# Kernel tuning notes

Measured on AMD Instinct MI355X. Metric: run time of the kernel, lower is better.

## Reference

```python
import jax, jax.numpy as jnp
import numpy as np

HIDDEN = 4096
N_HEADS = 32
N_KV_HEADS = 8
HEAD_DIM = HIDDEN // N_HEADS  # 128
GROUPS = N_HEADS // N_KV_HEADS  # 4
ROPE_BASE = 10000.0
BATCH, SEQ = 1, 2048


def _rope_cos_sin(position_ids, dim, base):
    # position_ids: [b, s] int -> cos/sin [b, s, dim]
    inv_freq = 1.0 / (base ** (jnp.arange(0, dim, 2, dtype=jnp.float32) / dim))  # [dim/2]
    freqs = position_ids.astype(jnp.float32)[..., None] * inv_freq  # [b, s, dim/2]
    emb = jnp.concatenate([freqs, freqs], axis=-1)  # [b, s, dim]
    return jnp.cos(emb), jnp.sin(emb)


def _rotate_half(x):
    x1, x2 = jnp.split(x, 2, axis=-1)
    return jnp.concatenate([-x2, x1], axis=-1)


def setup_inputs() -> dict:
    key = jax.random.key(0)
    ks = jax.random.split(key, 8)
    s = 0.02
    return {
        'hidden_states': jax.random.normal(ks[0], (BATCH, SEQ, HIDDEN), dtype=jnp.float32),
        'position_ids': jnp.broadcast_to(jnp.arange(SEQ, dtype=jnp.int64), (BATCH, SEQ)),
        'Wq': jax.random.normal(ks[1], (HIDDEN, N_HEADS * HEAD_DIM), dtype=jnp.float32) * s,
        'bq': jax.random.normal(ks[2], (N_HEADS * HEAD_DIM,), dtype=jnp.float32) * s,
        'Wk': jax.random.normal(ks[3], (HIDDEN, N_KV_HEADS * HEAD_DIM), dtype=jnp.float32) * s,
        'bk': jax.random.normal(ks[4], (N_KV_HEADS * HEAD_DIM,), dtype=jnp.float32) * s,
        'Wv': jax.random.normal(ks[5], (HIDDEN, N_KV_HEADS * HEAD_DIM), dtype=jnp.float32) * s,
        'bv': jax.random.normal(ks[6], (N_KV_HEADS * HEAD_DIM,), dtype=jnp.float32) * s,
        'Wo': jax.random.normal(ks[7], (HIDDEN, HIDDEN), dtype=jnp.float32) * s,
    }


def reference(hidden_states, position_ids, Wq, bq, Wk, bk, Wv, bv, Wo):
    b, s, _ = hidden_states.shape
    # QKV projections (bias=True for q/k/v per module)
    q = hidden_states @ Wq + bq  # [b, s, H*d]
    k = hidden_states @ Wk + bk  # [b, s, Hk*d]
    v = hidden_states @ Wv + bv  # [b, s, Hk*d]
    q = q.reshape(b, s, N_HEADS, HEAD_DIM)
    k = k.reshape(b, s, N_KV_HEADS, HEAD_DIM)
    v = v.reshape(b, s, N_KV_HEADS, HEAD_DIM)

    # RoPE gathered by position_ids
    cos, sin = _rope_cos_sin(position_ids, HEAD_DIM, ROPE_BASE)  # [b, s, d]
    cos = cos[:, :, None, :]
    sin = sin[:, :, None, :]
    q = q * cos + _rotate_half(q) * sin
    k = k * cos + _rotate_half(k) * sin

    # GQA causal attention: group query heads over shared kv heads
    qg = q.reshape(b, s, N_KV_HEADS, GROUPS, HEAD_DIM)
    scale = 1.0 / jnp.sqrt(jnp.asarray(HEAD_DIM, dtype=q.dtype))
    scores = jnp.einsum('bqhgd,bkhd->bhgqk', qg, k) * scale  # [b, Hk, g, s, s]
    causal = jnp.tril(jnp.ones((s, s), dtype=bool))
    scores = jnp.where(causal, scores, jnp.finfo(scores.dtype).min)
    probs = jax.nn.softmax(scores, axis=-1)
    out = jnp.einsum('bhgqk,bkhd->bqhgd', probs, v)  # [b, s, Hk, g, d]
    out = out.reshape(b, s, HIDDEN)
    return out @ Wo  # o_proj, bias=False
```

## Files before the change

### kernel.cpp

```cpp
#include <hip/hip_runtime.h>
#include <hip/hip_bf16.h>

typedef __hip_bfloat16 bf16;
typedef __attribute__((ext_vector_type(8))) __bf16 bf16x8;
typedef __attribute__((ext_vector_type(4))) float f32x4;

#define SEQ 2048
#define HID 4096
#define NH 32
#define NKV 8
#define HD 128
#define KVDIM 1024
#define QKVN 6144

#define MiB (1024 * 1024)

__device__ __forceinline__ void gl_lds16(const void* g, void* lds) {
  __builtin_amdgcn_global_load_lds((const __attribute__((address_space(1))) void*)g,
                                   (__attribute__((address_space(3))) void*)lds,
                                   16, 0, 0);
}

__device__ __forceinline__ float unplo(unsigned u) { return __uint_as_float(u << 16); }
__device__ __forceinline__ float unphi(unsigned u) { return __uint_as_float(u & 0xffff0000u); }
__device__ __forceinline__ unsigned packbf(float a, float b) {
  bf16 t[2] = {__float2bfloat16(a), __float2bfloat16(b)};
  return *reinterpret_cast<unsigned*>(t);
}

__global__ void cvt_kernel(const float* __restrict__ in, bf16* __restrict__ out, int n) {
  int i = (blockIdx.x * blockDim.x + threadIdx.x) * 4;
  if (i >= n) return;
  float4 v = *reinterpret_cast<const float4*>(in + i);
  bf16 o[4] = {__float2bfloat16(v.x), __float2bfloat16(v.y),
               __float2bfloat16(v.z), __float2bfloat16(v.w)};
  *reinterpret_cast<short4*>(out + i) = *reinterpret_cast<const short4*>(o);
}

__global__ void concat_bias_kernel(const float* __restrict__ bq, const float* __restrict__ bk,
                                   const float* __restrict__ bv, float* __restrict__ o) {
  int i = blockIdx.x * blockDim.x + threadIdx.x;
  if (i >= QKVN) return;
  o[i] = (i < HID) ? bq[i] : (i < HID + KVDIM ? bk[i - HID] : bv[i - HID - KVDIM]);
}

__global__ void transpose_all_kernel(const float* __restrict__ Wq, const float* __restrict__ Wk,
                                     const float* __restrict__ Wv, const float* __restrict__ Wo,
                                     bf16* __restrict__ Wqkvt, bf16* __restrict__ Wot) {
  __shared__ float tile[32][33];
  int t = blockIdx.x;
  const float* in;
  bf16* out;
  int si, xt, yt;
  if (t < 16384)      { in = Wq; out = Wqkvt;                           si = HID;   xt = t & 127; yt = t >> 7; }
  else if (t < 20480) { t -= 16384; in = Wk; out = Wqkvt + (size_t)HID * HID;           si = KVDIM; xt = t & 31; yt = t >> 5; }
  else if (t < 24576) { t -= 20480; in = Wv; out = Wqkvt + (size_t)(HID + KVDIM) * HID; si = KVDIM; xt = t & 31; yt = t >> 5; }
  else                { t -= 24576; in = Wo; out = Wot;                 si = HID;   xt = t & 127; yt = t >> 7; }
  int c0 = xt * 32, r0 = yt * 32;
  int tx = threadIdx.x, ty = threadIdx.y;
#pragma unroll
  for (int i = 0; i < 32; i += 8)
    tile[ty + i][tx] = in[(size_t)(r0 + ty + i) * si + (c0 + tx)];
  __syncthreads();
#pragma unroll
  for (int i = 0; i < 32; i += 8)
    out[(size_t)(c0 + ty + i) * HID + (r0 + tx)] = __float2bfloat16(tile[tx][ty + i]);
}

__global__ void postqkv_kernel(const bf16* __restrict__ Ch, bf16* __restrict__ Qb,
                               bf16* __restrict__ Kb, bf16* __restrict__ Vt) {
  __shared__ float tile[32][33];
  int b = blockIdx.x;
  int tid = threadIdx.x;
  if (b < 10240) {
    bool isQ = (b < 8192);
    int idx = (isQ ? b : b - 8192) * 256 + tid;
    int j = idx & 31;
    int h = (idx >> 5) & (isQ ? 31 : 7);
    int s = idx >> (isQ ? 10 : 8);
    size_t bi = (size_t)s * QKVN + (isQ ? 0 : HID) + h * HD;
    unsigned u1 = *reinterpret_cast<const unsigned*>(Ch + bi + 2 * j);
    unsigned u2 = *reinterpret_cast<const unsigned*>(Ch + bi + 64 + 2 * j);
    float x1a = unplo(u1), x1b = unphi(u1);
    float x2a = unplo(u2), x2b = unphi(u2);
    float inv0 = __expf(-(float)(2 * j) * 0.14391156831212787f);
    float inv1 = __expf(-(float)(2 * j + 1) * 0.14391156831212787f);
    float sn0, cs0, sn1, cs1;
    __sincosf((float)s * inv0, &sn0, &cs0);
    __sincosf((float)s * inv1, &sn1, &cs1);
    size_t bo = (size_t)s * (isQ ? HID : KVDIM) + h * HD;
    bf16* Ob = isQ ? Qb : Kb;
    *reinterpret_cast<unsigned*>(Ob + bo + 2 * j) =
        packbf(x1a * cs0 - x2a * sn0, x1b * cs1 - x2b * sn1);
    *reinterpret_cast<unsigned*>(Ob + bo + 64 + 2 * j) =
        packbf(x2a * cs0 + x1a * sn0, x2b * cs1 + x1b * sn1);
  } else {
    int t = b - 10240;
    int xt = t & 31, yt = t >> 5;
    int tx = tid & 31, ty = tid >> 5;
#pragma unroll
    for (int i = 0; i < 32; i += 8)
      tile[ty + i][tx] = __bfloat162float(Ch[(size_t)(yt * 32 + ty + i) * QKVN + (HID + KVDIM) + xt * 32 + tx]);
    __syncthreads();
#pragma unroll
    for (int i = 0; i < 32; i += 8)
      Vt[(size_t)(xt * 32 + ty + i) * SEQ + (yt * 32 + tx)] = __float2bfloat16(tile[tx][ty + i]);
  }
}

#define BARRIER() __builtin_amdgcn_s_barrier()
#define LGKM0()                                          \
  {                                                      \
    asm volatile("s_waitcnt lgkmcnt(0)" ::: "memory");   \
    __builtin_amdgcn_sched_barrier(0);                   \
  }
#define MFMA_ACC(d, x, y) d = __builtin_amdgcn_mfma_f32_16x16x32_bf16(x, y, d, 0, 0, 0)

__global__ __launch_bounds__(512, 2) void qkvgemm_kernel(
    const bf16* __restrict__ A,
    const bf16* __restrict__ Bt,
    const float* __restrict__ bias,
    bf16* __restrict__ Ch) {
  __shared__ bf16 lds[2][448 * 64];
  const int blk = blockIdx.x;
  const int sw = (blk & 7) * 32 + (blk >> 3);
  const int bx = sw & 31, by = sw >> 5;
  const int n0 = bx * 192;
  const int m0 = by * 256;
  const int tid = threadIdx.x;
  const int lane = tid & 63;
  const int w = tid >> 6;
  const int wr = w >> 2, wc = w & 3;
  const int hig = lane >> 4;
  const int nt = HID / 64;

#define QSTAGE_A(buf, t)                                                          \
  {                                                                               \
    _Pragma("unroll")                                                             \
    for (int _c = 0; _c < 4; ++_c) {                                              \
      int _row = _c * 64 + w * 8 + (lane >> 3);                                   \
      int _ch = (lane & 7) ^ ((lane >> 3) & 7);                                   \
      gl_lds16(A + (size_t)(m0 + _row) * HID + (size_t)(t) * 64 + _ch * 8,        \
               &lds[buf][(_c * 64 + w * 8) * 64]);                                \
    }                                                                             \
  }
#define QSTAGE_B(buf, t)                                                          \
  {                                                                               \
    _Pragma("unroll")                                                             \
    for (int _c = 0; _c < 3; ++_c) {                                              \
      int _row = _c * 64 + w * 8 + (lane >> 3);                                   \
      int _ch = (lane & 7) ^ ((lane >> 3) & 7);                                   \
      gl_lds16(Bt + (size_t)(n0 + _row) * HID + (size_t)(t) * 64 + _ch * 8,       \
               &lds[buf][(256 + _c * 64 + w * 8) * 64]);                          \
    }                                                                             \
  }

  auto rdA = [&](int cur, int mi, int ks) {
    int rr = wr * 128 + mi * 16 + (lane & 15);
    int byt = rr * 128 + (((ks * 32 + hig * 8) * 2) ^ ((rr & 7) << 4));
    return *reinterpret_cast<const bf16x8*>(
        reinterpret_cast<const char*>(&lds[cur][0]) + byt);
  };
  auto rdB = [&](int cur, int ni, int ks) {
    int rr = wc * 48 + ni * 16 + (lane & 15);
    int byt = 32768 + rr * 128 + (((ks * 32 + hig * 8) * 2) ^ ((rr & 7) << 4));
    return *reinterpret_cast<const bf16x8*>(
        reinterpret_cast<const char*>(&lds[cur][0]) + byt);
  };

  f32x4 acc[8][3];
  const f32x4 z = {0.f, 0.f, 0.f, 0.f};
#pragma unroll
  for (int i = 0; i < 8; ++i)
#pragma unroll
    for (int j = 0; j < 3; ++j) acc[i][j] = z;

  QSTAGE_A(0, 0); QSTAGE_B(0, 0);
  QSTAGE_B(1, 1);
  asm volatile("s_waitcnt vmcnt(3)" ::: "memory");
  BARRIER();

  bf16x8 a[4][2], b[3][2];
  int cur = 0;
  for (int t = 0; t < nt; ++t, cur ^= 1) {
#pragma unroll
    for (int mi = 0; mi < 4; ++mi) { a[mi][0] = rdA(cur, mi, 0); a[mi][1] = rdA(cur, mi, 1); }
#pragma unroll
    for (int ni = 0; ni < 3; ++ni) { b[ni][0] = rdB(cur, ni, 0); b[ni][1] = rdB(cur, ni, 1); }
    if (t + 1 < nt) QSTAGE_A(cur ^ 1, t + 1);
    LGKM0();
    __builtin_amdgcn_s_setprio(1);
#pragma unroll
    for (int mi = 0; mi < 4; ++mi)
#pragma unroll
      for (int ni = 0; ni < 3; ++ni) {
        MFMA_ACC(acc[mi][ni], a[mi][0], b[ni][0]);
        MFMA_ACC(acc[mi][ni], a[mi][1], b[ni][1]);
      }
    __builtin_amdgcn_s_setprio(0);
    BARRIER();
#pragma unroll
    for (int mi = 0; mi < 4; ++mi) { a[mi][0] = rdA(cur, mi + 4, 0); a[mi][1] = rdA(cur, mi + 4, 1); }
    if (t + 2 < nt) QSTAGE_B(cur, t + 2);
    LGKM0();
    __builtin_amdgcn_s_setprio(1);
#pragma unroll
    for (int mi = 0; mi < 4; ++mi)
#pragma unroll
      for (int ni = 0; ni < 3; ++ni) {
        MFMA_ACC(acc[mi + 4][ni], a[mi][0], b[ni][0]);
        MFMA_ACC(acc[mi + 4][ni], a[mi][1], b[ni][1]);
      }
    __builtin_amdgcn_s_setprio(0);
    if (t + 1 < nt) {
      if (t + 2 < nt) {
        asm volatile("s_waitcnt vmcnt(3)" ::: "memory");
      } else {
        asm volatile("s_waitcnt vmcnt(0)" ::: "memory");
      }
    }
    BARRIER();
  }

#pragma unroll
  for (int ni = 0; ni < 3; ++ni) {
    int col = n0 + wc * 48 + ni * 16 + (lane & 15);
    float bv = bias[col];
#pragma unroll
    for (int mi = 0; mi < 8; ++mi) {
      int rbase = m0 + wr * 128 + mi * 16 + hig * 4;
#pragma unroll
      for (int r = 0; r < 4; ++r)
        Ch[(size_t)(rbase + r) * QKVN + col] = __float2bfloat16(acc[mi][ni][r] + bv);
    }
  }
#undef QSTAGE_A
#undef QSTAGE_B
}

__global__ __launch_bounds__(512, 2) void wogemm_kernel(
    const bf16* __restrict__ A,
    const bf16* __restrict__ Bt,
    float* __restrict__ C) {
  __shared__ bf16 lds[2][3][128 * 64];
  const int blk = blockIdx.x;
  const int sw = (blk & 7) * 32 + (blk >> 3);
  const int n0 = (sw & 31) * 128;
  const int m0 = (sw >> 5) * 256;
  const int tid = threadIdx.x;
  const int lane = tid & 63;
  const int w = tid >> 6;
  const int wr = w >> 1, wc = w & 1;
  const int nt = HID / 64;

#define WSTAGE(buf, slot, t)                                                    \
  {                                                                             \
    const bf16* _s = ((slot) == 2) ? Bt : A;                                    \
    int _g0 = ((slot) == 2) ? n0 : (m0 + (slot) * 128);                         \
    _Pragma("unroll")                                                           \
    for (int _it = 0; _it < 2; ++_it) {                                         \
      int _row = w * 16 + _it * 8 + (lane >> 3);                                \
      int _ch = (lane & 7) ^ (_row & 7);                                        \
      gl_lds16(_s + (size_t)(_g0 + _row) * HID + (size_t)(t) * 64 + _ch * 8,    \
               &lds[buf][slot][(w * 16 + _it * 8) * 64]);                       \
    }                                                                           \
  }

  auto rdA = [&](int cur, int mi, int ks) {
    int rr = (wr & 1) * 64 + mi * 16 + (lane & 15);
    int byt = rr * 128 + (((ks * 32 + (lane >> 4) * 8) * 2) ^ ((rr & 7) << 4));
    return *reinterpret_cast<const bf16x8*>(
        reinterpret_cast<const char*>(&lds[cur][wr >> 1][0]) + byt);
  };
  auto rdB = [&](int cur, int ni, int ks) {
    int rr = wc * 64 + ni * 16 + (lane & 15);
    int byt = rr * 128 + (((ks * 32 + (lane >> 4) * 8) * 2) ^ ((rr & 7) << 4));
    return *reinterpret_cast<const bf16x8*>(
        reinterpret_cast<const char*>(&lds[cur][2][0]) + byt);
  };

  f32x4 acc[4][4];
  const f32x4 z = {0.f, 0.f, 0.f, 0.f};
#pragma unroll
  for (int i = 0; i < 4; ++i)
#pragma unroll
    for (int j = 0; j < 4; ++j) acc[i][j] = z;

  WSTAGE(0, 0, 0); WSTAGE(0, 1, 0); WSTAGE(0, 2, 0);
  WSTAGE(1, 2, 1);
  asm volatile("s_waitcnt vmcnt(2)" ::: "memory");
  BARRIER();

  bf16x8 a[2][2], b[4][2];
  int cur = 0;
  for (int t = 0; t < nt; ++t, cur ^= 1) {
#pragma unroll
    for (int mi = 0; mi < 2; ++mi) { a[mi][0] = rdA(cur, mi, 0); a[mi][1] = rdA(cur, mi, 1); }
#pragma unroll
    for (int ni = 0; ni < 4; ++ni) { b[ni][0] = rdB(cur, ni, 0); b[ni][1] = rdB(cur, ni, 1); }
    if (t + 1 < nt) { WSTAGE(cur ^ 1, 0, t + 1); WSTAGE(cur ^ 1, 1, t + 1); }
    LGKM0();
    __builtin_amdgcn_s_setprio(1);
#pragma unroll
    for (int mi = 0; mi < 2; ++mi)
#pragma unroll
      for (int ni = 0; ni < 4; ++ni) {
        MFMA_ACC(acc[mi][ni], a[mi][0], b[ni][0]);
        MFMA_ACC(acc[mi][ni], a[mi][1], b[ni][1]);
      }
    __builtin_amdgcn_s_setprio(0);
    BARRIER();
#pragma unroll
    for (int mi = 0; mi < 2; ++mi) { a[mi][0] = rdA(cur, mi + 2, 0); a[mi][1] = rdA(cur, mi + 2, 1); }
    if (t + 2 < nt) WSTAGE(cur, 2, t + 2);
    LGKM0();
    __builtin_amdgcn_s_setprio(1);
#pragma unroll
    for (int mi = 0; mi < 2; ++mi)
#pragma unroll
      for (int ni = 0; ni < 4; ++ni) {
        MFMA_ACC(acc[mi + 2][ni], a[mi][0], b[ni][0]);
        MFMA_ACC(acc[mi + 2][ni], a[mi][1], b[ni][1]);
      }
    __builtin_amdgcn_s_setprio(0);
    if (t + 1 < nt) {
      if (t + 2 < nt) {
        asm volatile("s_waitcnt vmcnt(2)" ::: "memory");
      } else {
        asm volatile("s_waitcnt vmcnt(0)" ::: "memory");
      }
    }
    BARRIER();
  }

#pragma unroll
  for (int ni = 0; ni < 4; ++ni) {
    int col = n0 + wc * 64 + ni * 16 + (lane & 15);
#pragma unroll
    for (int mi = 0; mi < 4; ++mi) {
      int rbase = m0 + wr * 64 + mi * 16 + (lane >> 4) * 4;
#pragma unroll
      for (int r = 0; r < 4; ++r)
        C[(size_t)(rbase + r) * HID + col] = acc[mi][ni][r];
    }
  }
#undef WSTAGE
}

__global__ __launch_bounds__(256) void attn_kernel(
    const bf16* __restrict__ Q, const bf16* __restrict__ Kb,
    const bf16* __restrict__ Vt, bf16* __restrict__ AO,
    float* __restrict__ Opart, float* __restrict__ Ml) {
  __shared__ bf16 Ks[64 * 128];
  __shared__ bf16 Vs[128 * 64];
  __shared__ bf16 Ps[4][16 * 64];
  const int tid = threadIdx.x, lane = tid & 63, w = tid >> 6;
  const int b = blockIdx.x;
  const int H = b & 31;
  const int tt = b >> 5;
  int qb, lo, hi, half;
  bool split;
  if (tt < 32) {
    qb = 16 + ((31 - tt) >> 1);
    half = tt & 1;
    int n = qb + 1, mid = n >> 1;
    lo = half ? mid : 0;
    hi = half ? n : mid;
    split = true;
  } else {
    qb = 47 - tt;
    half = 0;
    lo = 0;
    hi = qb + 1;
    split = false;
  }
  const int kvh = H >> 2;
  const int qw = qb * 64 + w * 16;
  const int hig = lane >> 4;
  const int q_loc = lane & 15;
  const int qa = qw + q_loc;

  bf16x8 aq[4];
#pragma unroll
  for (int kd = 0; kd < 4; ++kd) {
    int row = qw + q_loc;
    int d = kd * 32 + hig * 8;
    aq[kd] = *reinterpret_cast<const bf16x8*>(Q + (size_t)row * HID + H * HD + d);
  }

  float m_run = -1e30f, l_run = 0.0f;
  f32x4 o[8];
  const f32x4 z = {0.f, 0.f, 0.f, 0.f};
#pragma unroll
  for (int dt = 0; dt < 8; ++dt) o[dt] = z;

  const float scale = 0.08838834764831845f;

  for (int t = lo; t < hi; ++t) {
    int kvbase = t * 64;
#pragma unroll
    for (int it = 0; it < 4; ++it) {
      int c = w * 4 + it;
      int row = c * 4 + (lane >> 4);
      int sb = ((lane & 15) * 16) ^ ((row & 7) << 4);
      gl_lds16(Kb + (size_t)(kvbase + row) * KVDIM + kvh * HD + (sb >> 1), &Ks[c * 512]);
    }
#pragma unroll
    for (int it = 0; it < 4; ++it) {
      int c = w * 4 + it;
      int row = c * 8 + (lane >> 3);
      int sb = ((lane & 7) * 16) ^ ((row & 7) << 4);
      gl_lds16(Vt + (size_t)(kvh * HD + row) * SEQ + kvbase + (sb >> 1), &Vs[c * 512]);
    }
    __syncthreads();

    f32x4 sf[4];
#pragma unroll
    for (int j = 0; j < 4; ++j) sf[j] = z;
#pragma unroll
    for (int j = 0; j < 4; ++j) {
#pragma unroll
      for (int kd = 0; kd < 4; ++kd) {
        int r = j * 16 + q_loc;
        int byt = r * 256 + (((kd * 32 + hig * 8) * 2) ^ ((r & 7) << 4));
        bf16x8 kfr = *reinterpret_cast<const bf16x8*>(reinterpret_cast<const char*>(Ks) + byt);
        sf[j] = __builtin_amdgcn_mfma_f32_16x16x32_bf16(kfr, aq[kd], sf[j], 0, 0, 0);
      }
    }

    float vals[4][4];
    bool diag = (t == qb);
#pragma unroll
    for (int j = 0; j < 4; ++j)
#pragma unroll
      for (int r = 0; r < 4; ++r) {
        float v = sf[j][r] * scale;
        if (diag) {
          int ka = kvbase + j * 16 + hig * 4 + r;
          if (ka > qa) v = -1e30f;
        }
        vals[j][r] = v;
      }

    float m01 = fmaxf(fmaxf(vals[0][0], vals[0][1]), fmaxf(vals[0][2], vals[0][3]));
    float m23 = fmaxf(fmaxf(vals[1][0], vals[1][1]), fmaxf(vals[1][2], vals[1][3]));
    float m45 = fmaxf(fmaxf(vals[2][0], vals[2][1]), fmaxf(vals[2][2], vals[2][3]));
    float m67 = fmaxf(fmaxf(vals[3][0], vals[3][1]), fmaxf(vals[3][2], vals[3][3]));
    float m = fmaxf(fmaxf(m01, m23), fmaxf(m45, m67));
    m = fmaxf(m, __shfl_xor(m, 16));
    m = fmaxf(m, __shfl_xor(m, 32));
    float mn = fmaxf(m_run, m);
    float alpha = __expf(m_run - mn);
    m_run = mn;

    float p[4][4];
    float rs = 0.0f;
#pragma unroll
    for (int j = 0; j < 4; ++j)
#pragma unroll
      for (int r = 0; r < 4; ++r) {
        p[j][r] = __expf(vals[j][r] - mn);
        rs += p[j][r];
      }
    rs += __shfl_xor(rs, 16);
    rs += __shfl_xor(rs, 32);
    l_run = l_run * alpha + rs;

#pragma unroll
    for (int j = 0; j < 4; ++j) {
      bf16 tmp[4] = {__float2bfloat16(p[j][0]), __float2bfloat16(p[j][1]),
                     __float2bfloat16(p[j][2]), __float2bfloat16(p[j][3])};
      int coff = (j * 16 + hig * 4) * 2;
      int byt = q_loc * 128 + (coff ^ ((q_loc & 7) << 4));
      *reinterpret_cast<uint2*>(reinterpret_cast<char*>(&Ps[w][0]) + byt) =
          *reinterpret_cast<const uint2*>(tmp);
    }

#pragma unroll
    for (int r = 0; r < 4; ++r) {
      float alr = __shfl(alpha, hig * 4 + r);
#pragma unroll
      for (int dt = 0; dt < 8; ++dt) o[dt][r] *= alr;
    }

    bf16x8 pa[2];
#pragma unroll
    for (int ks = 0; ks < 2; ++ks) {
      int byt = q_loc * 128 + (((ks * 32 + hig * 8) * 2) ^ ((q_loc & 7) << 4));
      pa[ks] = *reinterpret_cast<const bf16x8*>(reinterpret_cast<const char*>(&Ps[w][0]) + byt);
    }
#pragma unroll
    for (int dt = 0; dt < 8; ++dt)
#pragma unroll
      for (int ks = 0; ks < 2; ++ks) {
        int vrow = dt * 16 + q_loc;
        int byt = vrow * 128 + (((ks * 32 + hig * 8) * 2) ^ ((vrow & 7) << 4));
        bf16x8 vb = *reinterpret_cast<const bf16x8*>(reinterpret_cast<const char*>(Vs) + byt);
        o[dt] = __builtin_amdgcn_mfma_f32_16x16x32_bf16(pa[ks], vb, o[dt], 0, 0, 0);
      }
    __syncthreads();
  }

  if (!split) {
#pragma unroll
    for (int r = 0; r < 4; ++r) {
      float li = __shfl(l_run, hig * 4 + r);
      float linv = 1.0f / li;
#pragma unroll
      for (int dt = 0; dt < 8; ++dt) {
        int qrow = qw + hig * 4 + r;
        int d = dt * 16 + q_loc;
        AO[(size_t)qrow * HID + H * HD + d] = __float2bfloat16(o[dt][r] * linv);
      }
    }
  } else {
    size_t pbase = ((size_t)(half * NH + H) * 1024);
#pragma unroll
    for (int dt = 0; dt < 8; ++dt)
#pragma unroll
      for (int r = 0; r < 4; ++r) {
        int qrow = qw + hig * 4 + r;
        int d = dt * 16 + q_loc;
        Opart[(pbase + (qrow - 1024)) * HD + d] = o[dt][r];
      }
    if (lane < 16) {
      Ml[(pbase + (qa - 1024)) * 2 + 0] = m_run;
      Ml[(pbase + (qa - 1024)) * 2 + 1] = l_run;
    }
  }
}

__global__ __launch_bounds__(256) void merge_kernel(
    const float* __restrict__ Opart, const float* __restrict__ Ml,
    bf16* __restrict__ AO) {
  int i = blockIdx.x * 256 + threadIdx.x;
  int dq = (i & 31) << 2;
  int row = (i >> 5) & 1023;
  int H = i >> 15;
  size_t b1 = (size_t)H * 1024 + row;
  size_t b2 = (size_t)(NH + H) * 1024 + row;
  float m1 = Ml[b1 * 2], l1 = Ml[b1 * 2 + 1];
  float m2 = Ml[b2 * 2], l2 = Ml[b2 * 2 + 1];
  float M = fmaxf(m1, m2);
  float w1 = __expf(m1 - M), w2 = __expf(m2 - M);
  float inv = 1.0f / (l1 * w1 + l2 * w2);
  float4 o1 = *reinterpret_cast<const float4*>(Opart + b1 * HD + dq);
  float4 o2 = *reinterpret_cast<const float4*>(Opart + b2 * HD + dq);
  bf16 o[4] = {__float2bfloat16((o1.x * w1 + o2.x * w2) * inv),
               __float2bfloat16((o1.y * w1 + o2.y * w2) * inv),
               __float2bfloat16((o1.z * w1 + o2.z * w2) * inv),
               __float2bfloat16((o1.w * w1 + o2.w * w2) * inv)};
  *reinterpret_cast<short4*>(AO + (size_t)(1024 + row) * HID + H * HD + dq) =
      *reinterpret_cast<const short4*>(o);
}

extern "C" void kernel_launch(void* const* d_in, const int* in_sizes, int n_in,
                              void* d_out, int out_size, void* d_ws, size_t ws_size,
                              hipStream_t stream) {
  const float* hidden = (const float*)d_in[0];
  const float* Wq = (const float*)d_in[2];
  const float* bq = (const float*)d_in[3];
  const float* Wk = (const float*)d_in[4];
  const float* bk = (const float*)d_in[5];
  const float* Wv = (const float*)d_in[6];
  const float* bv = (const float*)d_in[7];
  const float* Wo = (const float*)d_in[8];
  float* out = (float*)d_out;

  char* ws = (char*)d_ws;
  bf16*  Wqkvt  = (bf16*)(ws + (size_t)0 * MiB);
  bf16*  Xb     = (bf16*)(ws + (size_t)48 * MiB);
  bf16*  Cqkvh  = (bf16*)(ws + (size_t)64 * MiB);
  bf16*  Wot    = (bf16*)(ws + (size_t)88 * MiB);
  bf16*  Qb     = (bf16*)(ws + (size_t)120 * MiB);
  bf16*  Kb     = (bf16*)(ws + (size_t)136 * MiB);
  bf16*  Vt     = (bf16*)(ws + (size_t)140 * MiB);
  float* bqkv   = (float*)Qb;
  bf16*  AO     = Cqkvh;
  float* Opart  = (float*)Wqkvt;
  float* Ml     = (float*)(ws + (size_t)48 * MiB);

  cvt_kernel<<<(SEQ * HID) / 1024, 256, 0, stream>>>(hidden, Xb, SEQ * HID);
  concat_bias_kernel<<<QKVN / 256, 256, 0, stream>>>(bq, bk, bv, bqkv);
  transpose_all_kernel<<<40960, dim3(32, 8), 0, stream>>>(Wq, Wk, Wv, Wo, Wqkvt, Wot);

  qkvgemm_kernel<<<256, 512, 0, stream>>>(Xb, Wqkvt, bqkv, Cqkvh);

  postqkv_kernel<<<12288, 256, 0, stream>>>(Cqkvh, Qb, Kb, Vt);

  attn_kernel<<<1536, 256, 0, stream>>>(Qb, Kb, Vt, AO, Opart, Ml);
  merge_kernel<<<(NH * 1024 * 32) / 256, 256, 0, stream>>>(Opart, Ml, AO);

  wogemm_kernel<<<256, 512, 0, stream>>>(AO, Wot, out);
}
```

Before: 316.9 us.

## Double-buffer K/V tiles in attention kernel to overlap loads with MFMA

The attention kernel now keeps two LDS buffers for the K and V tiles. It issues the global-to-LDS loads for the next KV block before computing on the current one, and removes the barrier that waited for loads at the top of each iteration. The goal is to hide global memory latency behind the QK and PV MFMA work. The cost is doubled K/V shared memory, which can reduce how many blocks fit on each CU.

```diff
diff --git a/kernel.cpp b/kernel.cpp
--- a/kernel.cpp
+++ b/kernel.cpp
@@ -351,8 +351,8 @@
     const bf16* __restrict__ Q, const bf16* __restrict__ Kb,
     const bf16* __restrict__ Vt, bf16* __restrict__ AO,
     float* __restrict__ Opart, float* __restrict__ Ml) {
-  __shared__ bf16 Ks[64 * 128];
-  __shared__ bf16 Vs[128 * 64];
+  __shared__ bf16 Ks[2][64 * 128];
+  __shared__ bf16 Vs[2][128 * 64];
   __shared__ bf16 Ps[4][16 * 64];
   const int tid = threadIdx.x, lane = tid & 63, w = tid >> 6;
   const int b = blockIdx.x;
@@ -380,6 +380,27 @@
   const int q_loc = lane & 15;
   const int qa = qw + q_loc;
 
+#define STAGEKV(buf, t)                                                           \
+  {                                                                               \
+    int kvb = (t) * 64;                                                           \
+    _Pragma("unroll")                                                             \
+    for (int _it = 0; _it < 4; ++_it) {                                           \
+      int _c = w * 4 + _it;                                                       \
+      int _row = _c * 4 + (lane >> 4);                                            \
+      int _sb = ((lane & 15) * 16) ^ ((_row & 7) << 4);                           \
+      gl_lds16(Kb + (size_t)(kvb + _row) * KVDIM + kvh * HD + (_sb >> 1),         \
+               &Ks[buf][_c * 512]);                                               \
+    }                                                                             \
+    _Pragma("unroll")                                                             \
+    for (int _it = 0; _it < 4; ++_it) {                                           \
+      int _c = w * 4 + _it;                                                       \
+      int _row = _c * 8 + (lane >> 3);                                            \
+      int _sb = ((lane & 7) * 16) ^ ((_row & 7) << 4);                            \
+      gl_lds16(Vt + (size_t)(kvh * HD + _row) * SEQ + kvb + (_sb >> 1),           \
+               &Vs[buf][_c * 512]);                                               \
+    }                                                                             \
+  }
+
   bf16x8 aq[4];
 #pragma unroll
   for (int kd = 0; kd < 4; ++kd) {
@@ -396,24 +417,14 @@
 
   const float scale = 0.08838834764831845f;
 
+  STAGEKV(lo & 1, lo);
+  __syncthreads();
+
   for (int t = lo; t < hi; ++t) {
+    const int cur = t & 1;
+    if (t + 1 < hi) STAGEKV((t + 1) & 1, t + 1);
+
     int kvbase = t * 64;
-#pragma unroll
-    for (int it = 0; it < 4; ++it) {
-      int c = w * 4 + it;
-      int row = c * 4 + (lane >> 4);
-      int sb = ((lane & 15) * 16) ^ ((row & 7) << 4);
-      gl_lds16(Kb + (size_t)(kvbase + row) * KVDIM + kvh * HD + (sb >> 1), &Ks[c * 512]);
-    }
-#pragma unroll
-    for (int it = 0; it < 4; ++it) {
-      int c = w * 4 + it;
-      int row = c * 8 + (lane >> 3);
-      int sb = ((lane & 7) * 16) ^ ((row & 7) << 4);
-      gl_lds16(Vt + (size_t)(kvh * HD + row) * SEQ + kvbase + (sb >> 1), &Vs[c * 512]);
-    }
-    __syncthreads();
-
     f32x4 sf[4];
 #pragma unroll
     for (int j = 0; j < 4; ++j) sf[j] = z;
@@ -423,7 +434,8 @@
       for (int kd = 0; kd < 4; ++kd) {
         int r = j * 16 + q_loc;
         int byt = r * 256 + (((kd * 32 + hig * 8) * 2) ^ ((r & 7) << 4));
-        bf16x8 kfr = *reinterpret_cast<const bf16x8*>(reinterpret_cast<const char*>(Ks) + byt);
+        bf16x8 kfr = *reinterpret_cast<const bf16x8*>(
+            reinterpret_cast<const char*>(&Ks[cur][0]) + byt);
         sf[j] = __builtin_amdgcn_mfma_f32_16x16x32_bf16(kfr, aq[kd], sf[j], 0, 0, 0);
       }
     }
@@ -495,7 +507,8 @@
       for (int ks = 0; ks < 2; ++ks) {
         int vrow = dt * 16 + q_loc;
         int byt = vrow * 128 + (((ks * 32 + hig * 8) * 2) ^ ((vrow & 7) << 4));
-        bf16x8 vb = *reinterpret_cast<const bf16x8*>(reinterpret_cast<const char*>(Vs) + byt);
+        bf16x8 vb = *reinterpret_cast<const bf16x8*>(
+            reinterpret_cast<const char*>(&Vs[cur][0]) + byt);
         o[dt] = __builtin_amdgcn_mfma_f32_16x16x32_bf16(pa[ks], vb, o[dt], 0, 0, 0);
       }
     __syncthreads();
@@ -528,6 +541,7 @@
       Ml[(pbase + (qa - 1024)) * 2 + 1] = l_run;
     }
   }
+#undef STAGEKV
 }
 
 __global__ __launch_bounds__(256) void merge_kernel(
```

After: 325.7 us. 1.03x slower.
